# Kernel tuning notes

Hardware: AMD Instinct MI355X
Metric: run time of the kernel (lower is better)

The kernel has to match this reference:

```python
import jax, jax.numpy as jnp
import numpy as np

TAU = 0.1
POS_T = 0.5
NEG_T = 0.3
IOU_DIFF_T = 0.2


def setup_inputs() -> dict:
    key = jax.random.key(0)
    k1, k2, k3 = jax.random.split(key, 3)
    N, D = 8192, 256
    proposal_features = jax.random.normal(k1, (N, D), dtype=jnp.float32)
    proposal_ious = jax.random.uniform(k2, (N,), dtype=jnp.float32)
    # labels in {-1, 0..19}; -1 = background (filtered out by fg mask)
    proposal_labels = jax.random.randint(k3, (N,), -1, 20)
    return {
        "proposal_features": proposal_features,
        "proposal_ious": proposal_ious,
        "proposal_labels": proposal_labels,
    }


def reference(proposal_features, proposal_ious, proposal_labels):
    N = proposal_features.shape[0]
    fg = proposal_labels >= 0  # [N]

    # L2-normalize rows (F.normalize with eps=1e-12 clamp on norm)
    norm = jnp.sqrt(jnp.sum(proposal_features * proposal_features, axis=1, keepdims=True))
    f = proposal_features / jnp.maximum(norm, 1e-12)

    # [N, N] cosine similarity / temperature
    sim = jnp.matmul(f, f.T) / TAU

    same = proposal_labels[:, None] == proposal_labels[None, :]
    iou_i = proposal_ious[:, None]  # row proposal's IoU
    iou_j = proposal_ious[None, :]
    iou_mask = (iou_j > POS_T) & (iou_i > POS_T) & (jnp.abs(iou_j - iou_i) < IOU_DIFF_T)

    pair_fg = fg[:, None] & fg[None, :]  # both proposals foreground
    not_self = ~jnp.eye(N, dtype=bool)

    pos = same & iou_mask & pair_fg & not_self
    neg = (~same | (iou_i < NEG_T)) & pair_fg & not_self
    allm = pos | neg

    # per-row stabilized masked log-sum-exp ratio
    masked_sim = jnp.where(allm, sim, -jnp.inf)
    m = jnp.clip(jnp.max(masked_sim, axis=1), -20.0, 20.0)  # clamp as in torch code
    e = jnp.exp(masked_sim - m[:, None])  # zeros outside allm
    pos_sum = jnp.clip(jnp.sum(jnp.where(pos, e, 0.0), axis=1), 1e-6, 1e6)
    all_sum = jnp.clip(jnp.sum(e, axis=1), 1e-6, 1e6)
    loss_i = jnp.minimum(-jnp.log(pos_sum / all_sum), 10.0)

    # rows kept by the loop: fg with at least one pos and one neg
    valid = fg & jnp.any(pos, axis=1) & jnp.any(neg, axis=1)
    cnt = jnp.sum(valid)
    total = jnp.sum(jnp.where(valid, loss_i, 0.0))
    return jnp.where(cnt > 0, total / jnp.maximum(cnt, 1).astype(total.dtype), jnp.float32(0.0))
```

## Files before the change

### kernel.cpp

```cpp
#include <hip/hip_runtime.h>
#include <hip/hip_bf16.h>

#define N_ROWS 8192
#define DIM 256
#define R_BLK 64
#define C_CHUNK 512
#define TILE_C 32
#define N_CHUNKS 16
#define N_ITERS (C_CHUNK / TILE_C)
#define N_PBLK 512

typedef __attribute__((ext_vector_type(4))) float f32x4;
typedef __attribute__((ext_vector_type(8))) short bf16x8;

__device__ __forceinline__ void gload_lds16(const void* g, void* l) {
    using gv = const __attribute__((address_space(1))) void*;
    using sv = __attribute__((address_space(3))) void*;
    __builtin_amdgcn_global_load_lds((gv)g, (sv)l, 16, 0, 0);
}

__device__ __forceinline__ ushort f2bf(float v) {
    __hip_bfloat16 h = __float2bfloat16(v);
    return *reinterpret_cast<ushort*>(&h);
}

__global__ __launch_bounds__(256) void prep_kernel(const float* __restrict__ feat,
                                                   const float* __restrict__ ious,
                                                   const int* __restrict__ labels,
                                                   ushort* __restrict__ fhi,
                                                   int* __restrict__ raw,
                                                   int* __restrict__ cnt,
                                                   int* __restrict__ done) {
    if (blockIdx.x == 0 && threadIdx.x == 0) done[0] = 0;
    const int wid  = threadIdx.x >> 6;
    const int lane = threadIdx.x & 63;
#pragma unroll
    for (int r4 = 0; r4 < 4; ++r4) {
        const int row = blockIdx.x * 16 + r4 * 4 + wid;
        const float4 x = reinterpret_cast<const float4*>(feat + (size_t)row * DIM)[lane];
        float ss = x.x * x.x + x.y * x.y + x.z * x.z + x.w * x.w;
#pragma unroll
        for (int off = 32; off; off >>= 1) ss += __shfl_xor(ss, off);
        const float inv = 1.0f / fmaxf(sqrtf(ss), 1e-12f);
        ushort4 h;
        h.x = f2bf(x.x * inv); h.y = f2bf(x.y * inv);
        h.z = f2bf(x.z * inv); h.w = f2bf(x.w * inv);
        reinterpret_cast<ushort4*>(fhi + (size_t)row * DIM)[lane] = h;
    }
    if (threadIdx.x < 64) {
        const int row = blockIdx.x * 16 + (lane & 15);
        const bool act = (lane < 16) && (labels[row] >= 0) && (ious[row] > 0.5f);
        const unsigned long long mb = __ballot(act);
        const int off = __popcll(mb & ((1ull << lane) - 1ull));
        if (act) raw[blockIdx.x * 16 + off] = row;
        if (lane == 0) cnt[blockIdx.x] = __popcll(mb);
    }
}

__global__ __launch_bounds__(256, 4) void main_kernel(const ushort* __restrict__ fhi,
                                                      const float* __restrict__ ious,
                                                      const int* __restrict__ labels,
                                                      const int* __restrict__ raw,
                                                      const int* __restrict__ cnt,
                                                      float* __restrict__ ps_part,
                                                      float* __restrict__ as_part) {
    const int tid  = threadIdx.x;
    const int lane = tid & 63;

    __shared__ int sex[N_PBLK + 1];
    if (tid < 64) {
        int v[8], p[8];
        int lsum = 0;
#pragma unroll
        for (int k = 0; k < 8; ++k) { v[k] = cnt[lane * 8 + k]; p[k] = lsum; lsum += v[k]; }
        int inc = lsum;
#pragma unroll
        for (int off = 1; off < 64; off <<= 1) {
            const int t = __shfl_up(inc, off);
            if (lane >= off) inc += t;
        }
        const int base = inc - lsum;
        if (lane == 0) sex[0] = 0;
#pragma unroll
        for (int k = 0; k < 8; ++k) sex[lane * 8 + k + 1] = base + p[k] + v[k];
    }
    __syncthreads();
    const int nactive = sex[N_PBLK];

    const int bid   = blockIdx.x;
    const int rbase = (bid >> 4) * R_BLK;
    if (rbase >= nactive) return;

    const int chunk = bid & (N_CHUNKS - 1);
    const int c0    = chunk * C_CHUNK;

    const int w    = tid >> 6;
    const int lrow = lane & 15;
    const int kg   = lane >> 4;
    const int s0   = rbase + w * 16;

    auto slot2row = [&](int s) {
        int lo = 0, hi = N_PBLK;
#pragma unroll
        for (int step = 0; step < 9; ++step) {
            const int mid = (lo + hi) >> 1;
            if (sex[mid] <= s) lo = mid; else hi = mid;
        }
        return raw[lo * 16 + (s - sex[lo])];
    };

    __shared__ bf16x8 bt[2][1024];
    __shared__ int    lab_s[C_CHUNK];
    __shared__ float  iou_s[C_CHUNK];

#pragma unroll
    for (int i = tid; i < C_CHUNK; i += 256) {
        lab_s[i] = labels[c0 + i];
        iou_s[i] = ious[c0 + i];
    }

    bf16x8 av[8];
    {
        const int rowA = slot2row(min(s0 + lrow, nactive - 1));
        const ushort* pa = fhi + (size_t)rowA * DIM + kg * 8;
#pragma unroll
        for (int t = 0; t < 8; ++t) av[t] = *reinterpret_cast<const bf16x8*>(pa + t * 32);
    }

    int rowm[4]; int labi[4]; float ioui[4]; int livem = 0;
#pragma unroll
    for (int m = 0; m < 4; ++m) {
        const int slot = s0 + kg * 4 + m;
        const bool lv = slot < nactive;
        livem |= lv ? (1 << m) : 0;
        const int gi = slot2row(min(slot, nactive - 1));
        rowm[m] = gi;
        labi[m] = lv ? labels[gi] : -2;
        ioui[m] = ious[gi];
    }

    float ps[4] = {0.f,0.f,0.f,0.f}, as_[4] = {0.f,0.f,0.f,0.f};

    const char* fhib = (const char*)fhi;
    char* btb = (char*)&bt[0][0];
    auto stage = [&](int buf, int it) {
        const int jc = c0 + it * TILE_C;
#pragma unroll
        for (int iss = 0; iss < 4; ++iss) {
            const int L    = iss * 256 + tid;
            const int half = L >> 9;
            const int rem  = L & 511;
            const int t    = rem >> 6;
            const int lr   = (rem >> 2) & 15;
            const int kg2  = rem & 3;
            const char* src = fhib + (((size_t)(jc + half * 16 + lr)) << 9) + (kg2 * 16 + t * 64);
            char* dst = btb + buf * 16384 + iss * 4096 + tid * 16;
            gload_lds16(src, dst);
        }
    };

    stage(0, 0);
    __syncthreads();

    const float C1 = 14.42695041f;
    int cur = 0;
    for (int it = 0; it < N_ITERS; ++it) {
        if (it + 1 < N_ITERS) stage(cur ^ 1, it + 1);

        const int jcl = it * TILE_C;
        const int colg0 = c0 + jcl + lrow;
        const int colg1 = colg0 + 16;
        const int labj0 = lab_s[jcl + lrow];
        const int labj1 = lab_s[jcl + 16 + lrow];
        const float iouj0 = iou_s[jcl + lrow];
        const float iouj1 = iou_s[jcl + 16 + lrow];

        f32x4 acc0 = {0.f,0.f,0.f,0.f}, acc1 = {0.f,0.f,0.f,0.f};
        const char* lbase = btb + cur * 16384 + ((lrow * 4 + kg) << 4);
#pragma unroll
        for (int t = 0; t < 8; ++t) {
            bf16x8 b0 = *reinterpret_cast<const bf16x8*>(lbase + t * 1024);
            bf16x8 b1 = *reinterpret_cast<const bf16x8*>(lbase + 8192 + t * 1024);
            acc0 = __builtin_amdgcn_mfma_f32_16x16x32_bf16(av[t], b0, acc0, 0, 0, 0);
            acc1 = __builtin_amdgcn_mfma_f32_16x16x32_bf16(av[t], b1, acc1, 0, 0, 0);
        }

#pragma unroll
        for (int half = 0; half < 2; ++half) {
            const int colg = half ? colg1 : colg0;
            const int labj = half ? labj1 : labj0;
            const float iouj = half ? iouj1 : iouj0;
            const f32x4 acc = half ? acc1 : acc0;
            const bool fgj = labj >= 0;
            const bool hij = iouj > 0.5f;
#pragma unroll
            for (int m = 0; m < 4; ++m) {
                const bool same = (labi[m] == labj);
                const bool ioum = hij && (fabsf(iouj - ioui[m]) < 0.2f);
                const bool pf   = fgj && (rowm[m] != colg);
                const bool pos  = same && ioum && pf;
                const bool allm = pf && (ioum || !same);
                const float e = allm ? exp2f(fmaf(acc[m], C1, -C1)) : 0.0f;
                as_[m] += e;
                ps[m]  += pos ? e : 0.0f;
            }
        }
        asm volatile("s_waitcnt vmcnt(0)" ::: "memory");
        __builtin_amdgcn_s_barrier();
        __builtin_amdgcn_sched_barrier(0);
        cur ^= 1;
    }

#pragma unroll
    for (int off = 1; off < 16; off <<= 1) {
#pragma unroll
        for (int m = 0; m < 4; ++m) {
            ps[m]  += __shfl_xor(ps[m], off);
            as_[m] += __shfl_xor(as_[m], off);
        }
    }

    if (lrow == 0) {
#pragma unroll
        for (int m = 0; m < 4; ++m) {
            if ((livem >> m) & 1) {
                const int idx = chunk * N_ROWS + rowm[m];
                ps_part[idx] = ps[m];
                as_part[idx] = as_[m];
            }
        }
    }
}

__global__ __launch_bounds__(256) void combine_kernel(const float* __restrict__ ps_part,
                                                      const float* __restrict__ as_part,
                                                      const float* __restrict__ ious,
                                                      const int* __restrict__ labels,
                                                      float* __restrict__ partT,
                                                      float* __restrict__ partC,
                                                      int* __restrict__ done,
                                                      float* __restrict__ out) {
    const int tid = threadIdx.x;
    const int row = blockIdx.x * 256 + tid;
    const bool act = (labels[row] >= 0) && (ious[row] > 0.5f);
    float loss = 0.f, vld = 0.f;
    if (act) {
        float P = 0.f, A = 0.f;
#pragma unroll
        for (int c = 0; c < N_CHUNKS; ++c) {
            P += ps_part[c * N_ROWS + row];
            A += as_part[c * N_ROWS + row];
        }
        const float psc = fminf(fmaxf(P, 1e-6f), 1e6f);
        const float asc = fminf(fmaxf(A, 1e-6f), 1e6f);
        const bool valid = (P > 0.0f) && (A > P);
        loss = valid ? fminf(__logf(asc) - __logf(psc), 10.0f) : 0.0f;
        vld  = valid ? 1.0f : 0.0f;
    }
    float tl = loss, tc = vld;
#pragma unroll
    for (int off = 32; off; off >>= 1) { tl += __shfl_down(tl, off); tc += __shfl_down(tc, off); }
    __shared__ float sl[4], sc4[4];
    const int wid = tid >> 6;
    if ((tid & 63) == 0) { sl[wid] = tl; sc4[wid] = tc; }
    __syncthreads();
    if (tid == 0) {
        partT[blockIdx.x] = sl[0] + sl[1] + sl[2] + sl[3];
        partC[blockIdx.x] = sc4[0] + sc4[1] + sc4[2] + sc4[3];
        __threadfence();
        const int prev = atomicAdd(done, 1);
        if (prev == (int)gridDim.x - 1) {
            __threadfence();
            float T = 0.f, C = 0.f;
#pragma unroll
            for (int b = 0; b < N_ROWS / 256; ++b) { T += partT[b]; C += partC[b]; }
            out[0] = (C > 0.f) ? (T / C) : 0.0f;
        }
    }
}

extern "C" void kernel_launch(void* const* d_in, const int* in_sizes, int n_in,
                              void* d_out, int out_size, void* d_ws, size_t ws_size,
                              hipStream_t stream) {
    const float* feat   = (const float*)d_in[0];
    const float* ious   = (const float*)d_in[1];
    const int*   labels = (const int*)d_in[2];
    float* out = (float*)d_out;

    ushort* fhi = (ushort*)d_ws;
    float*  ps_part = (float*)(fhi + (size_t)N_ROWS * DIM);
    float*  as_part = ps_part + (size_t)N_CHUNKS * N_ROWS;
    int*    raw  = (int*)(as_part + (size_t)N_CHUNKS * N_ROWS);
    int*    cnt  = raw + N_ROWS;
    int*    done = cnt + N_PBLK;
    float*  partT = (float*)(done + 1);
    float*  partC = partT + (N_ROWS / 256);

    prep_kernel<<<N_PBLK, 256, 0, stream>>>(feat, ious, labels, fhi, raw, cnt, done);
    main_kernel<<<(N_ROWS / R_BLK) * N_CHUNKS, 256, 0, stream>>>(fhi, ious, labels,
                                                                 raw, cnt, ps_part, as_part);
    combine_kernel<<<N_ROWS / 256, 256, 0, stream>>>(ps_part, as_part, ious, labels,
                                                     partT, partC, done, out);
}
```

Before: 49.80 us.

## Fuse combine step into main kernel via per-row-block last-arriver reduction

```diff
diff --git a/kernel.cpp b/kernel.cpp
--- a/kernel.cpp
+++ b/kernel.cpp
@@ -9,6 +9,7 @@
 #define N_CHUNKS 16
 #define N_ITERS (C_CHUNK / TILE_C)
 #define N_PBLK 512
+#define N_RBLK 128
 
 typedef __attribute__((ext_vector_type(4))) float f32x4;
 typedef __attribute__((ext_vector_type(8))) short bf16x8;
@@ -30,8 +31,12 @@
                                                    ushort* __restrict__ fhi,
                                                    int* __restrict__ raw,
                                                    int* __restrict__ cnt,
+                                                   int* __restrict__ rb_cnt,
                                                    int* __restrict__ done) {
-    if (blockIdx.x == 0 && threadIdx.x == 0) done[0] = 0;
+    if (threadIdx.x == 0) {
+        if (blockIdx.x < N_RBLK) rb_cnt[blockIdx.x] = 0;
+        if (blockIdx.x == 0) done[0] = 0;
+    }
     const int wid  = threadIdx.x >> 6;
     const int lane = threadIdx.x & 63;
 #pragma unroll
@@ -63,7 +68,12 @@
                                                       const int* __restrict__ raw,
                                                       const int* __restrict__ cnt,
                                                       float* __restrict__ ps_part,
-                                                      float* __restrict__ as_part) {
+                                                      float* __restrict__ as_part,
+                                                      int* __restrict__ rb_cnt,
+                                                      int* __restrict__ done,
+                                                      float* __restrict__ partT,
+                                                      float* __restrict__ partC,
+                                                      float* __restrict__ out) {
     const int tid  = threadIdx.x;
     const int lane = tid & 63;
 
@@ -87,8 +97,13 @@
     __syncthreads();
     const int nactive = sex[N_PBLK];
 
-    const int bid   = blockIdx.x;
-    const int rbase = (bid >> 4) * R_BLK;
+    const int bid    = blockIdx.x;
+    const int rowblk = bid >> 4;
+    const int rbase  = rowblk * R_BLK;
+    if (nactive == 0) {
+        if (bid == 0 && tid == 0) out[0] = 0.0f;
+        return;
+    }
     if (rbase >= nactive) return;
 
     const int chunk = bid & (N_CHUNKS - 1);
@@ -230,51 +245,49 @@
             }
         }
     }
-}
-
-__global__ __launch_bounds__(256) void combine_kernel(const float* __restrict__ ps_part,
-                                                      const float* __restrict__ as_part,
-                                                      const float* __restrict__ ious,
-                                                      const int* __restrict__ labels,
-                                                      float* __restrict__ partT,
-                                                      float* __restrict__ partC,
-                                                      int* __restrict__ done,
-                                                      float* __restrict__ out) {
-    const int tid = threadIdx.x;
-    const int row = blockIdx.x * 256 + tid;
-    const bool act = (labels[row] >= 0) && (ious[row] > 0.5f);
-    float loss = 0.f, vld = 0.f;
-    if (act) {
-        float P = 0.f, A = 0.f;
-#pragma unroll
-        for (int c = 0; c < N_CHUNKS; ++c) {
-            P += ps_part[c * N_ROWS + row];
-            A += as_part[c * N_ROWS + row];
-        }
-        const float psc = fminf(fmaxf(P, 1e-6f), 1e6f);
-        const float asc = fminf(fmaxf(A, 1e-6f), 1e6f);
-        const bool valid = (P > 0.0f) && (A > P);
-        loss = valid ? fminf(__logf(asc) - __logf(psc), 10.0f) : 0.0f;
-        vld  = valid ? 1.0f : 0.0f;
-    }
-    float tl = loss, tc = vld;
-#pragma unroll
-    for (int off = 32; off; off >>= 1) { tl += __shfl_down(tl, off); tc += __shfl_down(tc, off); }
-    __shared__ float sl[4], sc4[4];
-    const int wid = tid >> 6;
-    if ((tid & 63) == 0) { sl[wid] = tl; sc4[wid] = tc; }
+
+    __shared__ int amLast;
+    __threadfence();
     __syncthreads();
-    if (tid == 0) {
-        partT[blockIdx.x] = sl[0] + sl[1] + sl[2] + sl[3];
-        partC[blockIdx.x] = sc4[0] + sc4[1] + sc4[2] + sc4[3];
+    if (tid == 0) amLast = (atomicAdd(&rb_cnt[rowblk], 1) == N_CHUNKS - 1);
+    __syncthreads();
+    if (amLast) {
         __threadfence();
-        const int prev = atomicAdd(done, 1);
-        if (prev == (int)gridDim.x - 1) {
-            __threadfence();
-            float T = 0.f, C = 0.f;
-#pragma unroll
-            for (int b = 0; b < N_ROWS / 256; ++b) { T += partT[b]; C += partC[b]; }
-            out[0] = (C > 0.f) ? (T / C) : 0.0f;
+        float loss = 0.f, vld = 0.f;
+        if (tid < 64) {
+            const int slot = rbase + tid;
+            if (slot < nactive) {
+                const int row = slot2row(slot);
+                float P = 0.f, A = 0.f;
+#pragma unroll
+                for (int c = 0; c < N_CHUNKS; ++c) {
+                    P += ps_part[c * N_ROWS + row];
+                    A += as_part[c * N_ROWS + row];
+                }
+                const float psc = fminf(fmaxf(P, 1e-6f), 1e6f);
+                const float asc = fminf(fmaxf(A, 1e-6f), 1e6f);
+                const bool valid = (P > 0.0f) && (A > P);
+                loss = valid ? fminf(__logf(asc) - __logf(psc), 10.0f) : 0.0f;
+                vld  = valid ? 1.0f : 0.0f;
+            }
+#pragma unroll
+            for (int off = 32; off; off >>= 1) {
+                loss += __shfl_down(loss, off);
+                vld  += __shfl_down(vld, off);
+            }
+            if (tid == 0) {
+                partT[rowblk] = loss;
+                partC[rowblk] = vld;
+                __threadfence();
+                const int nrb = (nactive + R_BLK - 1) / R_BLK;
+                const int prev = atomicAdd(done, 1);
+                if (prev == nrb - 1) {
+                    __threadfence();
+                    float T = 0.f, C = 0.f;
+                    for (int b = 0; b < nrb; ++b) { T += partT[b]; C += partC[b]; }
+                    out[0] = (C > 0.f) ? (T / C) : 0.0f;
+                }
+            }
         }
     }
 }
@@ -292,13 +305,13 @@
     float*  as_part = ps_part + (size_t)N_CHUNKS * N_ROWS;
     int*    raw  = (int*)(as_part + (size_t)N_CHUNKS * N_ROWS);
     int*    cnt  = raw + N_ROWS;
-    int*    done = cnt + N_PBLK;
+    int*    rb_cnt = cnt + N_PBLK;
+    int*    done = rb_cnt + N_RBLK;
     float*  partT = (float*)(done + 1);
-    float*  partC = partT + (N_ROWS / 256);
-
-    prep_kernel<<<N_PBLK, 256, 0, stream>>>(feat, ious, labels, fhi, raw, cnt, done);
+    float*  partC = partT + N_RBLK;
+
+    prep_kernel<<<N_PBLK, 256, 0, stream>>>(feat, ious, labels, fhi, raw, cnt, rb_cnt, done);
     main_kernel<<<(N_ROWS / R_BLK) * N_CHUNKS, 256, 0, stream>>>(fhi, ious, labels,
-                                                                 raw, cnt, ps_part, as_part);
-    combine_kernel<<<N_ROWS / 256, 256, 0, stream>>>(ps_part, as_part, ious, labels,
-                                                     partT, partC, done, out);
-}
+                                                                 raw, cnt, ps_part, as_part,
+                                                                 rb_cnt, done, partT, partC, out);
+}
```

New measurement: 160.6 us. +222.5%, slower.
